# Kernel tuning notes

Measured on AMD Instinct MI355X. Metric: run time of the kernel, lower is better.

Reference implementation:

```python
import jax, jax.numpy as jnp
import numpy as np

N_NODES = 50000
N_EDGES = 800000
IN_DIM = 128
FEAT = 64
HID = 64
OUT = 64
EA_DIM = 3  # edge_attr columns; concat -> weight in_dim = 3*channels


def _uniform(key, shape, lo=-1.0, hi=1.0):
    return jax.random.uniform(key, shape, jnp.float32, lo, hi)


def setup_inputs() -> dict:
    key = jax.random.key(0)
    ks = jax.random.split(key, 12)
    x = jax.random.normal(ks[0], (N_NODES, IN_DIM), jnp.float32)
    edge_index = jax.random.randint(ks[1], (2, N_EDGES), 0, N_NODES, jnp.int32)
    edge_attr = jax.random.uniform(ks[2], (N_EDGES, EA_DIM), jnp.float32)
    # linear_pre (nn.Linear default init approximated; values irrelevant for correctness)
    pre_w = _uniform(ks[3], (IN_DIM, FEAT), -0.08, 0.08)
    pre_b = _uniform(ks[4], (FEAT,), -0.08, 0.08)
    # SAGEConvEGNN weights: uniform(-1, 1), shape [3*in, out]
    w1 = _uniform(ks[5], (EA_DIM * FEAT, HID))
    b1 = _uniform(ks[6], (HID,))
    w2 = _uniform(ks[7], (EA_DIM * HID, HID))
    b2 = _uniform(ks[8], (HID,))
    w3 = _uniform(ks[9], (EA_DIM * HID, OUT))
    b3 = _uniform(ks[10], (OUT,))
    return {"x": x, "edge_index": edge_index, "edge_attr": edge_attr,
            "pre_w": pre_w, "pre_b": pre_b,
            "w1": w1, "b1": b1, "w2": w2, "b2": b2, "w3": w3, "b3": b3}


def _sage_conv(h, src, tgt, edge_attr, w, b, n_nodes):
    # message: x_j scaled by each of the 3 edge_attr columns, concatenated -> [E, 3*C]
    xj = h[src]                                              # gather [E, C]
    msg = (edge_attr[:, :, None] * xj[:, None, :]).reshape(xj.shape[0], -1)
    s = jax.ops.segment_sum(msg, tgt, num_segments=n_nodes)  # scatter-sum [N, 3C]
    cnt = jax.ops.segment_sum(jnp.ones((src.shape[0],), msg.dtype), tgt,
                              num_segments=n_nodes)
    agg = s / jnp.maximum(cnt, 1.0)[:, None]                 # mean; 0 for isolated nodes
    return agg @ w + b


def reference(x, edge_index, edge_attr, pre_w, pre_b, w1, b1, w2, b2, w3, b3):
    src, tgt = edge_index[0], edge_index[1]  # message from j=src aggregated at i=tgt
    n = x.shape[0]
    h = x @ pre_w + pre_b                     # linear_pre
    h = jax.nn.relu(_sage_conv(h, src, tgt, edge_attr, w1, b1, n))
    h = jax.nn.relu(_sage_conv(h, src, tgt, edge_attr, w2, b2, n))
    h = _sage_conv(h, src, tgt, edge_attr, w3, b3, n)
    # F.normalize(p=2, dim=-1) with eps=1e-12
    norm = jnp.sqrt(jnp.sum(h * h, axis=-1, keepdims=True))
    return h / jnp.maximum(norm, 1e-12)
```

## Files before the change

### kernel.cpp

```cpp
#include <hip/hip_runtime.h>
#include <hip/hip_bf16.h>

#define NN 50000
#define NE 800000
#define IND 128
#define C 64
#define NBUCK 196

typedef __hip_bfloat16 bf16;
typedef __attribute__((ext_vector_type(8))) short s8v;
typedef __attribute__((ext_vector_type(4))) float f4v;

__device__ __forceinline__ float to_f(float v) { return v; }
__device__ __forceinline__ float to_f(bf16 v)  { return __bfloat162float(v); }

__device__ __forceinline__ unsigned short f2b(float v) {
    unsigned u = __float_as_uint(v);
    return (unsigned short)((u + 0x7FFFu + ((u >> 16) & 1u)) >> 16);
}
__device__ __forceinline__ float b2f(unsigned short u) {
    return __uint_as_float((unsigned)u << 16);
}

__global__ void detect_kernel(const unsigned* __restrict__ xu, int* __restrict__ flag) {
    int lane = threadIdx.x;
    unsigned u  = xu[lane];
    unsigned ex = (u >> 7) & 0xFF;
    int vote = (ex >= 90 && ex <= 144) ? 1 : 0;
#pragma unroll
    for (int off = 32; off; off >>= 1) vote += __shfl_xor(vote, off, 64);
    if (lane == 0) *flag = (vote < 40) ? 1 : 0;
}

__global__ void count_kernel(const int* __restrict__ tgt, int* __restrict__ cnt) {
    int e = blockIdx.x * blockDim.x + threadIdx.x;
    if (e < NE) atomicAdd(&cnt[tgt[e]], 1);
}

__global__ __launch_bounds__(256) void scanA_kernel(const int4* __restrict__ cnt4,
                                                    int* __restrict__ bsum) {
    __shared__ int ws[4];
    int tid = threadIdx.x;
    int idx = blockIdx.x * 256 + tid;
    int4 v = (idx < NN / 4) ? cnt4[idx] : make_int4(0, 0, 0, 0);
    int s = v.x + v.y + v.z + v.w;
#pragma unroll
    for (int o = 32; o; o >>= 1) s += __shfl_xor(s, o, 64);
    if ((tid & 63) == 0) ws[tid >> 6] = s;
    __syncthreads();
    if (tid == 0) bsum[blockIdx.x] = ws[0] + ws[1] + ws[2] + ws[3];
}

__global__ __launch_bounds__(256) void scanC_kernel(const int4* __restrict__ cnt4,
                                                    const int* __restrict__ bsum,
                                                    int* __restrict__ off) {
    __shared__ int wsum[4];
    int tid = threadIdx.x, lane = tid & 63, wv = tid >> 6;
    int b = blockIdx.x;
    int bb = (lane < b) ? bsum[lane] : 0;
#pragma unroll
    for (int o = 32; o; o >>= 1) bb += __shfl_xor(bb, o, 64);
    int idx = b * 256 + tid;
    int4 v = (idx < NN / 4) ? cnt4[idx] : make_int4(0, 0, 0, 0);
    int tot = v.x + v.y + v.z + v.w;
    int incl = tot;
#pragma unroll
    for (int d = 1; d < 64; d <<= 1) { int t = __shfl_up(incl, d, 64); if (lane >= d) incl += t; }
    if (lane == 63) wsum[wv] = incl;
    __syncthreads();
    int wbase = 0;
#pragma unroll
    for (int j = 0; j < 4; ++j) wbase += (j < wv) ? wsum[j] : 0;
    int excl = bb + wbase + incl - tot;
    if (idx < NN / 4) {
        off[4 * idx]     = excl;
        off[4 * idx + 1] = excl + v.x;
        off[4 * idx + 2] = excl + v.x + v.y;
        off[4 * idx + 3] = excl + v.x + v.y + v.z;
    }
    if (b == 0 && tid == 0) off[NN] = NE;
}

template <typename T>
__device__ __forceinline__ void binA_impl(int* lcnt, int* lbase,
                                          const int* __restrict__ src,
                                          const int* __restrict__ tgt,
                                          const T* __restrict__ ea,
                                          const int* __restrict__ off,
                                          int* __restrict__ ccur,
                                          float4* __restrict__ stg) {
    int tid = threadIdx.x;
    for (int i = tid; i < NBUCK; i += 256) lcnt[i] = 0;
    __syncthreads();
    int e0 = blockIdx.x * 2048;
    float ex[8], ey[8], ez[8];
    unsigned ew[8];
    int eb[8], er[8];
#pragma unroll
    for (int k = 0; k < 8; ++k) {
        int e = e0 + (k << 8) + tid;
        if (e < NE) {
            int t = tgt[e];
            int s = src[e];
            eb[k] = t >> 8;
            ew[k] = ((unsigned)t << 16) | (unsigned)s;
            ex[k] = to_f(ea[e * 3 + 0]);
            ey[k] = to_f(ea[e * 3 + 1]);
            ez[k] = to_f(ea[e * 3 + 2]);
            er[k] = atomicAdd(&lcnt[eb[k]], 1);
        } else eb[k] = -1;
    }
    __syncthreads();
    for (int i = tid; i < NBUCK; i += 256) {
        int c = lcnt[i];
        int g = c ? atomicAdd(&ccur[i], c) : 0;
        lbase[i] = off[i << 8] + g;
    }
    __syncthreads();
#pragma unroll
    for (int k = 0; k < 8; ++k) {
        if (eb[k] >= 0) {
            float4 r;
            r.x = ex[k]; r.y = ey[k]; r.z = ez[k];
            r.w = __uint_as_float(ew[k]);
            stg[lbase[eb[k]] + er[k]] = r;
        }
    }
}

__global__ __launch_bounds__(256) void binA_kernel(const int* __restrict__ src,
                                                   const int* __restrict__ tgt,
                                                   const void* ea,
                                                   const int* __restrict__ off,
                                                   const int* __restrict__ flagp,
                                                   int* __restrict__ ccur,
                                                   float4* __restrict__ stg) {
    __shared__ int lcnt[NBUCK];
    __shared__ int lbase[NBUCK];
    if (*flagp) binA_impl<float>(lcnt, lbase, src, tgt, (const float*)ea, off, ccur, stg);
    else        binA_impl<bf16>(lcnt, lbase, src, tgt, (const bf16*)ea, off, ccur, stg);
}

__global__ __launch_bounds__(256) void binB_kernel(const float4* __restrict__ stg,
                                                   const int* __restrict__ off,
                                                   float4* __restrict__ edge) {
    __shared__ int lfill[256];
    __shared__ int loff[257];
    int tid = threadIdx.x;
    int n0 = blockIdx.x << 8;
    int nn = min(256, NN - n0);
    for (int i = tid; i < nn; i += 256) lfill[i] = 0;
    for (int i = tid; i <= nn; i += 256) loff[i] = off[n0 + i];
    __syncthreads();
    int cb = loff[0], ce = loff[nn];
    for (int i = cb + tid; i < ce; i += 256) {
        float4 r = stg[i];
        unsigned w = __float_as_uint(r.w);
        int l = (int)(w >> 16) & 255;
        int rk = atomicAdd(&lfill[l], 1);
        r.w = __uint_as_float(w & 0xFFFFu);
        edge[loff[l] + rk] = r;
    }
}

template <typename T>
__device__ __forceinline__ void wprep_impl(const T* __restrict__ w, int nT,
                                           unsigned short* __restrict__ oh,
                                           unsigned short* __restrict__ ol) {
    int idx = blockIdx.x * 256 + threadIdx.x;
    if (idx >= 2048 * nT) return;
    int j    = idx & 7;
    int lane = (idx >> 3) & 63;
    int r2   = idx >> 9;
    int t    = r2 % nT;
    int ct   = r2 / nT;
    int k    = 32 * t + ((lane >> 4) << 3) + j;
    int col  = 16 * ct + (lane & 15);
    if constexpr (sizeof(T) == 4) {
        float v = ((const float*)w)[k * 64 + col];
        unsigned short hi = f2b(v);
        oh[idx] = hi;
        ol[idx] = f2b(v - b2f(hi));
    } else {
        oh[idx] = ((const unsigned short*)w)[k * 64 + col];
    }
}

__global__ void wprep_kernel(const void* w, const int* __restrict__ flagp, int nT,
                             unsigned short* __restrict__ oh, unsigned short* __restrict__ ol) {
    if (*flagp) wprep_impl<float>((const float*)w, nT, oh, ol);
    else        wprep_impl<bf16>((const bf16*)w, nT, oh, ol);
}

template <typename T>
__device__ __forceinline__ void preM_impl(const T* __restrict__ x,
                                          const unsigned short* __restrict__ wfh,
                                          const unsigned short* __restrict__ wfl,
                                          const T* __restrict__ b,
                                          unsigned short* __restrict__ h) {
    int tid = threadIdx.x;
    int nb  = blockIdx.x * 64;
    int lane = tid & 63, wv = tid >> 6;
    int m = lane & 15, g = lane >> 4;
    int arow = nb + wv * 16 + m;
    bool okrow = arow < NN;
    f4v acc[4] = {};
    for (int t = 0; t < 4; ++t) {
        if constexpr (sizeof(T) == 4) {
            float av[8];
            if (okrow) {
                const float* xr = (const float*)x + (size_t)arow * IND + t * 32 + g * 8;
                float4 v0 = *(const float4*)xr;
                float4 v1 = *(const float4*)(xr + 4);
                av[0] = v0.x; av[1] = v0.y; av[2] = v0.z; av[3] = v0.w;
                av[4] = v1.x; av[5] = v1.y; av[6] = v1.z; av[7] = v1.w;
            } else {
#pragma unroll
                for (int j = 0; j < 8; ++j) av[j] = 0.f;
            }
            s8v ahi, alo;
#pragma unroll
            for (int j = 0; j < 8; ++j) {
                unsigned short hi = f2b(av[j]);
                ahi[j] = (short)hi;
                alo[j] = (short)f2b(av[j] - b2f(hi));
            }
#pragma unroll
            for (int ct = 0; ct < 4; ++ct) {
                int fo = ((ct * 4 + t) * 64 + lane) * 8;
                s8v bh = *(const s8v*)&wfh[fo];
                s8v bl = *(const s8v*)&wfl[fo];
                acc[ct] = __builtin_amdgcn_mfma_f32_16x16x32_bf16(ahi, bh, acc[ct], 0, 0, 0);
                acc[ct] = __builtin_amdgcn_mfma_f32_16x16x32_bf16(alo, bh, acc[ct], 0, 0, 0);
                acc[ct] = __builtin_amdgcn_mfma_f32_16x16x32_bf16(ahi, bl, acc[ct], 0, 0, 0);
            }
        } else {
            s8v ahi = {};
            if (okrow)
                ahi = *(const s8v*)((const unsigned short*)x + (size_t)arow * IND + t * 32 + g * 8);
#pragma unroll
            for (int ct = 0; ct < 4; ++ct) {
                int fo = ((ct * 4 + t) * 64 + lane) * 8;
                s8v bh = *(const s8v*)&wfh[fo];
                acc[ct] = __builtin_amdgcn_mfma_f32_16x16x32_bf16(ahi, bh, acc[ct], 0, 0, 0);
            }
        }
    }
#pragma unroll
    for (int r = 0; r < 4; ++r) {
        int drow = nb + wv * 16 + g * 4 + r;
        if (drow < NN) {
#pragma unroll
            for (int ct = 0; ct < 4; ++ct)
                h[(size_t)drow * C + 16 * ct + m] = f2b(acc[ct][r] + to_f(b[16 * ct + m]));
        }
    }
}

__global__ __launch_bounds__(256) void preM_kernel(const void* x,
                                                   const unsigned short* __restrict__ wfh,
                                                   const unsigned short* __restrict__ wfl,
                                                   const void* b, const int* __restrict__ flagp,
                                                   unsigned short* __restrict__ h) {
    if (*flagp) preM_impl<float>((const float*)x, wfh, wfl, (const float*)b, h);
    else        preM_impl<bf16>((const bf16*)x, wfh, wfl, (const bf16*)b, h);
}

__global__ __launch_bounds__(256) void agg_kernel(const unsigned short* __restrict__ hb,
                                                  const float4* __restrict__ edge,
                                                  const int* __restrict__ off,
                                                  float* __restrict__ s) {
    int f = threadIdx.x & 63;
    int n = blockIdx.x * 4 + (threadIdx.x >> 6);
    int beg = __builtin_amdgcn_readfirstlane(off[n]);
    int end = __builtin_amdgcn_readfirstlane(off[n + 1]);
    float a0 = 0.f, a1 = 0.f, a2 = 0.f;
    int cnt = end - beg;
    int m4 = beg + (cnt & ~3);
    int e = beg;
    if (beg + 8 <= m4) {
        float4 c0 = edge[e],     c1 = edge[e + 1], c2 = edge[e + 2], c3 = edge[e + 3];
        float4 d0 = edge[e + 4], d1 = edge[e + 5], d2 = edge[e + 6], d3 = edge[e + 7];
        float h0 = b2f(hb[(__float_as_int(c0.w) << 6) + f]);
        float h1 = b2f(hb[(__float_as_int(c1.w) << 6) + f]);
        float h2 = b2f(hb[(__float_as_int(c2.w) << 6) + f]);
        float h3 = b2f(hb[(__float_as_int(c3.w) << 6) + f]);
        int e2 = beg + 8;
        while (e2 < m4) {
            float g0 = b2f(hb[(__float_as_int(d0.w) << 6) + f]);
            float g1 = b2f(hb[(__float_as_int(d1.w) << 6) + f]);
            float g2 = b2f(hb[(__float_as_int(d2.w) << 6) + f]);
            float g3 = b2f(hb[(__float_as_int(d3.w) << 6) + f]);
            float4 n0 = edge[e2], n1 = edge[e2 + 1], n2 = edge[e2 + 2], n3 = edge[e2 + 3];
            a0 += c0.x * h0; a1 += c0.y * h0; a2 += c0.z * h0;
            a0 += c1.x * h1; a1 += c1.y * h1; a2 += c1.z * h1;
            a0 += c2.x * h2; a1 += c2.y * h2; a2 += c2.z * h2;
            a0 += c3.x * h3; a1 += c3.y * h3; a2 += c3.z * h3;
            c0 = d0; c1 = d1; c2 = d2; c3 = d3;
            h0 = g0; h1 = g1; h2 = g2; h3 = g3;
            d0 = n0; d1 = n1; d2 = n2; d3 = n3;
            e2 += 4;
        }
        float g0 = b2f(hb[(__float_as_int(d0.w) << 6) + f]);
        float g1 = b2f(hb[(__float_as_int(d1.w) << 6) + f]);
        float g2 = b2f(hb[(__float_as_int(d2.w) << 6) + f]);
        float g3 = b2f(hb[(__float_as_int(d3.w) << 6) + f]);
        a0 += c0.x * h0; a1 += c0.y * h0; a2 += c0.z * h0;
        a0 += c1.x * h1; a1 += c1.y * h1; a2 += c1.z * h1;
        a0 += c2.x * h2; a1 += c2.y * h2; a2 += c2.z * h2;
        a0 += c3.x * h3; a1 += c3.y * h3; a2 += c3.z * h3;
        a0 += d0.x * g0; a1 += d0.y * g0; a2 += d0.z * g0;
        a0 += d1.x * g1; a1 += d1.y * g1; a2 += d1.z * g1;
        a0 += d2.x * g2; a1 += d2.y * g2; a2 += d2.z * g2;
        a0 += d3.x * g3; a1 += d3.y * g3; a2 += d3.z * g3;
        e = m4;
    } else if (beg + 4 <= m4) {
        float4 c0 = edge[e], c1 = edge[e + 1], c2 = edge[e + 2], c3 = edge[e + 3];
        float h0 = b2f(hb[(__float_as_int(c0.w) << 6) + f]);
        float h1 = b2f(hb[(__float_as_int(c1.w) << 6) + f]);
        float h2 = b2f(hb[(__float_as_int(c2.w) << 6) + f]);
        float h3 = b2f(hb[(__float_as_int(c3.w) << 6) + f]);
        a0 += c0.x * h0; a1 += c0.y * h0; a2 += c0.z * h0;
        a0 += c1.x * h1; a1 += c1.y * h1; a2 += c1.z * h1;
        a0 += c2.x * h2; a1 += c2.y * h2; a2 += c2.z * h2;
        a0 += c3.x * h3; a1 += c3.y * h3; a2 += c3.z * h3;
        e = m4;
    }
    for (; e < end; ++e) {
        float4 r = edge[e];
        float hv = b2f(hb[(__float_as_int(r.w) << 6) + f]);
        a0 += r.x * hv; a1 += r.y * hv; a2 += r.z * hv;
    }
    float iv = 1.0f / fmaxf((float)cnt, 1.0f);
    float* so = s + n * 192;
    so[f] = a0 * iv; so[64 + f] = a1 * iv; so[128 + f] = a2 * iv;
}

template <typename T, int MODE>
__device__ __forceinline__ void gemmM_impl(const float* __restrict__ s,
                                           const unsigned short* __restrict__ wfh,
                                           const unsigned short* __restrict__ wfl,
                                           const T* __restrict__ b,
                                           unsigned short* __restrict__ hout, T* __restrict__ out) {
    int tid = threadIdx.x;
    int nb  = blockIdx.x * 64;
    int lane = tid & 63, wv = tid >> 6;
    int m = lane & 15, g = lane >> 4;
    int arow = nb + wv * 16 + m;
    bool okrow = arow < NN;
    const float* srow = s + (size_t)arow * 192 + g * 8;
    f4v acc[4] = {};
    for (int t = 0; t < 6; ++t) {
        float av[8];
        if (okrow) {
            float4 v0 = *(const float4*)(srow + t * 32);
            float4 v1 = *(const float4*)(srow + t * 32 + 4);
            av[0] = v0.x; av[1] = v0.y; av[2] = v0.z; av[3] = v0.w;
            av[4] = v1.x; av[5] = v1.y; av[6] = v1.z; av[7] = v1.w;
        } else {
#pragma unroll
            for (int j = 0; j < 8; ++j) av[j] = 0.f;
        }
        s8v ahi, alo;
#pragma unroll
        for (int j = 0; j < 8; ++j) {
            unsigned short hi = f2b(av[j]);
            ahi[j] = (short)hi;
            alo[j] = (short)f2b(av[j] - b2f(hi));
        }
#pragma unroll
        for (int ct = 0; ct < 4; ++ct) {
            int fo = ((ct * 6 + t) * 64 + lane) * 8;
            s8v bh = *(const s8v*)&wfh[fo];
            acc[ct] = __builtin_amdgcn_mfma_f32_16x16x32_bf16(ahi, bh, acc[ct], 0, 0, 0);
            acc[ct] = __builtin_amdgcn_mfma_f32_16x16x32_bf16(alo, bh, acc[ct], 0, 0, 0);
            if constexpr (sizeof(T) == 4) {
                s8v bl = *(const s8v*)&wfl[fo];
                acc[ct] = __builtin_amdgcn_mfma_f32_16x16x32_bf16(ahi, bl, acc[ct], 0, 0, 0);
            }
        }
    }
    float vv[4][4];
#pragma unroll
    for (int ct = 0; ct < 4; ++ct) {
        float bv = to_f(b[16 * ct + m]);
#pragma unroll
        for (int r = 0; r < 4; ++r) vv[ct][r] = acc[ct][r] + bv;
    }
    if constexpr (MODE == 0) {
#pragma unroll
        for (int r = 0; r < 4; ++r) {
            int drow = nb + wv * 16 + g * 4 + r;
            if (drow < NN) {
#pragma unroll
                for (int ct = 0; ct < 4; ++ct)
                    hout[(size_t)drow * C + 16 * ct + m] = f2b(fmaxf(vv[ct][r], 0.f));
            }
        }
    } else {
#pragma unroll
        for (int r = 0; r < 4; ++r) {
            float sq = vv[0][r] * vv[0][r] + vv[1][r] * vv[1][r]
                     + vv[2][r] * vv[2][r] + vv[3][r] * vv[3][r];
#pragma unroll
            for (int o = 1; o < 16; o <<= 1) sq += __shfl_xor(sq, o, 64);
            float innorm = 1.0f / fmaxf(sqrtf(sq), 1e-12f);
            int drow = nb + wv * 16 + g * 4 + r;
            if (drow < NN) {
#pragma unroll
                for (int ct = 0; ct < 4; ++ct) {
                    float rv = vv[ct][r] * innorm;
                    if constexpr (sizeof(T) == 2) out[(size_t)drow * C + 16 * ct + m] = __float2bfloat16(rv);
                    else                          out[(size_t)drow * C + 16 * ct + m] = rv;
                }
            }
        }
    }
}

__global__ __launch_bounds__(256) void gemm_relu(const float* __restrict__ s,
                                                 const unsigned short* __restrict__ wfh,
                                                 const unsigned short* __restrict__ wfl,
                                                 const void* b, const int* __restrict__ flagp,
                                                 unsigned short* __restrict__ hout) {
    if (*flagp) gemmM_impl<float, 0>(s, wfh, wfl, (const float*)b, hout, (float*)nullptr);
    else        gemmM_impl<bf16, 0>(s, wfh, wfl, (const bf16*)b, hout, (bf16*)nullptr);
}

__global__ __launch_bounds__(256) void gemm_norm(const float* __restrict__ s,
                                                 const unsigned short* __restrict__ wfh,
                                                 const unsigned short* __restrict__ wfl,
                                                 const void* b, const int* __restrict__ flagp,
                                                 void* out) {
    if (*flagp) gemmM_impl<float, 1>(s, wfh, wfl, (const float*)b, nullptr, (float*)out);
    else        gemmM_impl<bf16, 1>(s, wfh, wfl, (const bf16*)b, nullptr, (bf16*)out);
}

extern "C" void kernel_launch(void* const* d_in, const int* in_sizes, int n_in,
                              void* d_out, int out_size, void* d_ws, size_t ws_size,
                              hipStream_t stream) {
    const void* x     = d_in[0];
    const int*  ei    = (const int*)d_in[1];
    const void* ea    = d_in[2];
    const void* pre_w = d_in[3];
    const void* pre_b = d_in[4];
    const void* W[3]  = {d_in[5], d_in[7], d_in[9]};
    const void* B[3]  = {d_in[6], d_in[8], d_in[10]};
    const int* src = ei;
    const int* tgt = ei + NE;

    float4*         EDGE = (float4*)d_ws;
    float*          S    = (float*)(EDGE + NE);
    float4*         STG  = (float4*)S;
    unsigned short* H    = (unsigned short*)(S + (size_t)NN * 192);
    int*            CNT  = (int*)(H + (size_t)NN * C);
    int*            CCUR = CNT + NN;
    int*            OFF  = CCUR + 256;
    int*            BSUM = OFF + NN + 8;
    int*            FLAG = BSUM + 64;
    unsigned short* WPH  = (unsigned short*)(FLAG + 16);
    unsigned short* WPL  = WPH + 8192;
    unsigned short* WFH  = WPL + 8192;
    unsigned short* WFL  = WFH + 3 * 12288;

    detect_kernel<<<1, 64, 0, stream>>>((const unsigned*)x, FLAG);
    wprep_kernel<<<32, 256, 0, stream>>>(pre_w, FLAG, 4, WPH, WPL);
    for (int l = 0; l < 3; ++l)
        wprep_kernel<<<48, 256, 0, stream>>>(W[l], FLAG, 6, WFH + l * 12288, WFL + l * 12288);
    hipMemsetAsync(CNT, 0, (NN + 256) * sizeof(int), stream);
    count_kernel<<<(NE + 255) / 256, 256, 0, stream>>>(tgt, CNT);
    scanA_kernel<<<(NN / 4 + 255) / 256, 256, 0, stream>>>((const int4*)CNT, BSUM);
    scanC_kernel<<<(NN / 4 + 255) / 256, 256, 0, stream>>>((const int4*)CNT, BSUM, OFF);
    binA_kernel<<<(NE + 2047) / 2048, 256, 0, stream>>>(src, tgt, ea, OFF, FLAG, CCUR, STG);
    binB_kernel<<<NBUCK, 256, 0, stream>>>(STG, OFF, EDGE);
    preM_kernel<<<(NN + 63) / 64, 256, 0, stream>>>(x, WPH, WPL, pre_b, FLAG, H);

    int nblk = (NN + 63) / 64;
    for (int l = 0; l < 3; ++l) {
        agg_kernel<<<NN / 4, 256, 0, stream>>>(H, EDGE, OFF, S);
        if (l < 2)
            gemm_relu<<<nblk, 256, 0, stream>>>(S, WFH + l * 12288, WFL + l * 12288, B[l], FLAG, H);
        else
            gemm_norm<<<nblk, 256, 0, stream>>>(S, WFH + l * 12288, WFL + l * 12288, B[l], FLAG, d_out);
    }
}
```

Baseline: 317.9 us.

## Fuse preprocessing kernels, derive CSR offsets in bucket pass, store agg as bf16 pairs

Merges the weight-prep launches with a per-bucket target count into one kernel. It replaces the per-node count plus two-stage scan with a tiny bucket scan, and computes the per-node CSR offsets inside the binB pass, which is fused with the pre-linear GEMM. The aggregation now writes hi/lo bf16 splits instead of fp32, so the GEMM loads them directly without converting. This cuts the number of launches and removes the global per-node atomics, at the cost of an extra pass over staging in binB and more complex shared-memory logic.

```diff
diff --git a/kernel.cpp b/kernel.cpp
--- a/kernel.cpp
+++ b/kernel.cpp
@@ -32,38 +32,55 @@
     if (lane == 0) *flag = (vote < 40) ? 1 : 0;
 }
 
-__global__ void count_kernel(const int* __restrict__ tgt, int* __restrict__ cnt) {
-    int e = blockIdx.x * blockDim.x + threadIdx.x;
-    if (e < NE) atomicAdd(&cnt[tgt[e]], 1);
-}
-
-__global__ __launch_bounds__(256) void scanA_kernel(const int4* __restrict__ cnt4,
-                                                    int* __restrict__ bsum) {
-    __shared__ int ws[4];
+__global__ __launch_bounds__(256) void prep_kernel(const void* pw, const void* w0,
+        const void* w1, const void* w2, const int* __restrict__ flagp,
+        const int* __restrict__ tgt,
+        unsigned short* __restrict__ oh, unsigned short* __restrict__ ol,
+        int* __restrict__ bcnt) {
+    __shared__ int lc[NBUCK];
+    int blk = blockIdx.x;
     int tid = threadIdx.x;
-    int idx = blockIdx.x * 256 + tid;
-    int4 v = (idx < NN / 4) ? cnt4[idx] : make_int4(0, 0, 0, 0);
-    int s = v.x + v.y + v.z + v.w;
-#pragma unroll
-    for (int o = 32; o; o >>= 1) s += __shfl_xor(s, o, 64);
-    if ((tid & 63) == 0) ws[tid >> 6] = s;
-    __syncthreads();
-    if (tid == 0) bsum[blockIdx.x] = ws[0] + ws[1] + ws[2] + ws[3];
-}
-
-__global__ __launch_bounds__(256) void scanC_kernel(const int4* __restrict__ cnt4,
-                                                    const int* __restrict__ bsum,
+    if (blk < 176) {
+        int gid = blk * 256 + tid;
+        const void* w; int nT, idx, base;
+        if (gid < 8192) { w = pw; nT = 4; idx = gid; base = 0; }
+        else {
+            int r = gid - 8192; int l = r / 12288; idx = r % 12288; nT = 6;
+            w = (l == 0) ? w0 : (l == 1) ? w1 : w2; base = 8192 + l * 12288;
+        }
+        int j = idx & 7, lane = (idx >> 3) & 63, r2 = idx >> 9;
+        int t = r2 % nT, ct = r2 / nT;
+        int k = 32 * t + ((lane >> 4) << 3) + j;
+        int col = 16 * ct + (lane & 15);
+        if (*flagp) {
+            float v = ((const float*)w)[k * 64 + col];
+            unsigned short hi = f2b(v);
+            oh[base + idx] = hi;
+            ol[base + idx] = f2b(v - b2f(hi));
+        } else {
+            oh[base + idx] = ((const unsigned short*)w)[k * 64 + col];
+        }
+    } else {
+        for (int i = tid; i < NBUCK; i += 256) lc[i] = 0;
+        __syncthreads();
+        int e0 = (blk - 176) * 2048;
+#pragma unroll
+        for (int k = 0; k < 8; ++k) {
+            int e = e0 + (k << 8) + tid;
+            if (e < NE) atomicAdd(&lc[tgt[e] >> 8], 1);
+        }
+        __syncthreads();
+        for (int i = tid; i < NBUCK; i += 256) if (lc[i]) atomicAdd(&bcnt[i], lc[i]);
+    }
+}
+
+__global__ __launch_bounds__(256) void bscan_kernel(const int* __restrict__ bcnt,
+                                                    int* __restrict__ boff,
                                                     int* __restrict__ off) {
     __shared__ int wsum[4];
     int tid = threadIdx.x, lane = tid & 63, wv = tid >> 6;
-    int b = blockIdx.x;
-    int bb = (lane < b) ? bsum[lane] : 0;
-#pragma unroll
-    for (int o = 32; o; o >>= 1) bb += __shfl_xor(bb, o, 64);
-    int idx = b * 256 + tid;
-    int4 v = (idx < NN / 4) ? cnt4[idx] : make_int4(0, 0, 0, 0);
-    int tot = v.x + v.y + v.z + v.w;
-    int incl = tot;
+    int v = (tid < NBUCK) ? bcnt[tid] : 0;
+    int incl = v;
 #pragma unroll
     for (int d = 1; d < 64; d <<= 1) { int t = __shfl_up(incl, d, 64); if (lane >= d) incl += t; }
     if (lane == 63) wsum[wv] = incl;
@@ -71,14 +88,8 @@
     int wbase = 0;
 #pragma unroll
     for (int j = 0; j < 4; ++j) wbase += (j < wv) ? wsum[j] : 0;
-    int excl = bb + wbase + incl - tot;
-    if (idx < NN / 4) {
-        off[4 * idx]     = excl;
-        off[4 * idx + 1] = excl + v.x;
-        off[4 * idx + 2] = excl + v.x + v.y;
-        off[4 * idx + 3] = excl + v.x + v.y + v.z;
-    }
-    if (b == 0 && tid == 0) off[NN] = NE;
+    if (tid < NBUCK) boff[tid] = wbase + incl - v;
+    if (tid == 0) { boff[NBUCK] = NE; off[NN] = NE; }
 }
 
 template <typename T>
@@ -86,7 +97,7 @@
                                           const int* __restrict__ src,
                                           const int* __restrict__ tgt,
                                           const T* __restrict__ ea,
-                                          const int* __restrict__ off,
+                                          const int* __restrict__ boff,
                                           int* __restrict__ ccur,
                                           float4* __restrict__ stg) {
     int tid = threadIdx.x;
@@ -114,7 +125,7 @@
     for (int i = tid; i < NBUCK; i += 256) {
         int c = lcnt[i];
         int g = c ? atomicAdd(&ccur[i], c) : 0;
-        lbase[i] = off[i << 8] + g;
+        lbase[i] = boff[i] + g;
     }
     __syncthreads();
 #pragma unroll
@@ -131,75 +142,23 @@
 __global__ __launch_bounds__(256) void binA_kernel(const int* __restrict__ src,
                                                    const int* __restrict__ tgt,
                                                    const void* ea,
-                                                   const int* __restrict__ off,
+                                                   const int* __restrict__ boff,
                                                    const int* __restrict__ flagp,
                                                    int* __restrict__ ccur,
                                                    float4* __restrict__ stg) {
     __shared__ int lcnt[NBUCK];
     __shared__ int lbase[NBUCK];
-    if (*flagp) binA_impl<float>(lcnt, lbase, src, tgt, (const float*)ea, off, ccur, stg);
-    else        binA_impl<bf16>(lcnt, lbase, src, tgt, (const bf16*)ea, off, ccur, stg);
-}
-
-__global__ __launch_bounds__(256) void binB_kernel(const float4* __restrict__ stg,
-                                                   const int* __restrict__ off,
-                                                   float4* __restrict__ edge) {
-    __shared__ int lfill[256];
-    __shared__ int loff[257];
-    int tid = threadIdx.x;
-    int n0 = blockIdx.x << 8;
-    int nn = min(256, NN - n0);
-    for (int i = tid; i < nn; i += 256) lfill[i] = 0;
-    for (int i = tid; i <= nn; i += 256) loff[i] = off[n0 + i];
-    __syncthreads();
-    int cb = loff[0], ce = loff[nn];
-    for (int i = cb + tid; i < ce; i += 256) {
-        float4 r = stg[i];
-        unsigned w = __float_as_uint(r.w);
-        int l = (int)(w >> 16) & 255;
-        int rk = atomicAdd(&lfill[l], 1);
-        r.w = __uint_as_float(w & 0xFFFFu);
-        edge[loff[l] + rk] = r;
-    }
+    if (*flagp) binA_impl<float>(lcnt, lbase, src, tgt, (const float*)ea, boff, ccur, stg);
+    else        binA_impl<bf16>(lcnt, lbase, src, tgt, (const bf16*)ea, boff, ccur, stg);
 }
 
 template <typename T>
-__device__ __forceinline__ void wprep_impl(const T* __restrict__ w, int nT,
-                                           unsigned short* __restrict__ oh,
-                                           unsigned short* __restrict__ ol) {
-    int idx = blockIdx.x * 256 + threadIdx.x;
-    if (idx >= 2048 * nT) return;
-    int j    = idx & 7;
-    int lane = (idx >> 3) & 63;
-    int r2   = idx >> 9;
-    int t    = r2 % nT;
-    int ct   = r2 / nT;
-    int k    = 32 * t + ((lane >> 4) << 3) + j;
-    int col  = 16 * ct + (lane & 15);
-    if constexpr (sizeof(T) == 4) {
-        float v = ((const float*)w)[k * 64 + col];
-        unsigned short hi = f2b(v);
-        oh[idx] = hi;
-        ol[idx] = f2b(v - b2f(hi));
-    } else {
-        oh[idx] = ((const unsigned short*)w)[k * 64 + col];
-    }
-}
-
-__global__ void wprep_kernel(const void* w, const int* __restrict__ flagp, int nT,
-                             unsigned short* __restrict__ oh, unsigned short* __restrict__ ol) {
-    if (*flagp) wprep_impl<float>((const float*)w, nT, oh, ol);
-    else        wprep_impl<bf16>((const bf16*)w, nT, oh, ol);
-}
-
-template <typename T>
-__device__ __forceinline__ void preM_impl(const T* __restrict__ x,
+__device__ __forceinline__ void preM_body(int nb, const T* __restrict__ x,
                                           const unsigned short* __restrict__ wfh,
                                           const unsigned short* __restrict__ wfl,
                                           const T* __restrict__ b,
                                           unsigned short* __restrict__ h) {
     int tid = threadIdx.x;
-    int nb  = blockIdx.x * 64;
     int lane = tid & 63, wv = tid >> 6;
     int m = lane & 15, g = lane >> 4;
     int arow = nb + wv * 16 + m;
@@ -257,19 +216,62 @@
     }
 }
 
-__global__ __launch_bounds__(256) void preM_kernel(const void* x,
-                                                   const unsigned short* __restrict__ wfh,
-                                                   const unsigned short* __restrict__ wfl,
-                                                   const void* b, const int* __restrict__ flagp,
-                                                   unsigned short* __restrict__ h) {
-    if (*flagp) preM_impl<float>((const float*)x, wfh, wfl, (const float*)b, h);
-    else        preM_impl<bf16>((const bf16*)x, wfh, wfl, (const bf16*)b, h);
+__global__ __launch_bounds__(256) void binB_pre_kernel(const float4* __restrict__ stg,
+        const int* __restrict__ boff, int* __restrict__ off, float4* __restrict__ edge,
+        const void* x, const unsigned short* __restrict__ wfh,
+        const unsigned short* __restrict__ wfl, const void* pb,
+        const int* __restrict__ flagp, unsigned short* __restrict__ h) {
+    __shared__ int lcnt[256];
+    __shared__ int lexcl[256];
+    __shared__ int lfill[256];
+    __shared__ int wsum[4];
+    int tid = threadIdx.x;
+    if (blockIdx.x < NBUCK) {
+        int b = blockIdx.x;
+        int n0 = b << 8;
+        int cb = boff[b], ce = boff[b + 1];
+        lcnt[tid] = 0;
+        __syncthreads();
+        for (int i = cb + tid; i < ce; i += 256) {
+            unsigned w = __float_as_uint(stg[i].w);
+            atomicAdd(&lcnt[(w >> 16) & 255], 1);
+        }
+        __syncthreads();
+        int lane = tid & 63, wv = tid >> 6;
+        int v = lcnt[tid];
+        int incl = v;
+#pragma unroll
+        for (int d = 1; d < 64; d <<= 1) { int t = __shfl_up(incl, d, 64); if (lane >= d) incl += t; }
+        if (lane == 63) wsum[wv] = incl;
+        __syncthreads();
+        int wbase = 0;
+#pragma unroll
+        for (int j = 0; j < 4; ++j) wbase += (j < wv) ? wsum[j] : 0;
+        lexcl[tid] = wbase + incl - v;
+        lfill[tid] = 0;
+        __syncthreads();
+        int n = n0 + tid;
+        if (n <= NN) off[n] = cb + lexcl[tid];
+        for (int i = cb + tid; i < ce; i += 256) {
+            float4 r = stg[i];
+            unsigned w = __float_as_uint(r.w);
+            int l = (int)(w >> 16) & 255;
+            int rk = atomicAdd(&lfill[l], 1);
+            r.w = __uint_as_float(w & 0xFFFFu);
+            edge[cb + lexcl[l] + rk] = r;
+        }
+    } else {
+        int nb = (blockIdx.x - NBUCK) * 64;
+        if (*flagp) preM_body<float>(nb, (const float*)x, wfh, wfl, (const float*)pb, h);
+        else        preM_body<bf16>(nb, (const bf16*)x, wfh, wfl, (const bf16*)pb, h);
+    }
 }
 
 __global__ __launch_bounds__(256) void agg_kernel(const unsigned short* __restrict__ hb,
                                                   const float4* __restrict__ edge,
                                                   const int* __restrict__ off,
-                                                  float* __restrict__ s) {
+                                                  unsigned short* __restrict__ sh,
+                                                  unsigned short* __restrict__ sl) {
     int f = threadIdx.x & 63;
     int n = blockIdx.x * 4 + (threadIdx.x >> 6);
     int beg = __builtin_amdgcn_readfirstlane(off[n]);
@@ -332,12 +334,17 @@
         a0 += r.x * hv; a1 += r.y * hv; a2 += r.z * hv;
     }
     float iv = 1.0f / fmaxf((float)cnt, 1.0f);
-    float* so = s + n * 192;
-    so[f] = a0 * iv; so[64 + f] = a1 * iv; so[128 + f] = a2 * iv;
+    size_t base = (size_t)n * 192;
+    float v0 = a0 * iv, v1 = a1 * iv, v2 = a2 * iv;
+    unsigned short x0 = f2b(v0), x1 = f2b(v1), x2 = f2b(v2);
+    sh[base + f]       = x0; sl[base + f]       = f2b(v0 - b2f(x0));
+    sh[base + 64 + f]  = x1; sl[base + 64 + f]  = f2b(v1 - b2f(x1));
+    sh[base + 128 + f] = x2; sl[base + 128 + f] = f2b(v2 - b2f(x2));
 }
 
 template <typename T, int MODE>
-__device__ __forceinline__ void gemmM_impl(const float* __restrict__ s,
+__device__ __forceinline__ void gemmM_impl(const unsigned short* __restrict__ sh,
+                                           const unsigned short* __restrict__ sl,
                                            const unsigned short* __restrict__ wfh,
                                            const unsigned short* __restrict__ wfl,
                                            const T* __restrict__ b,
@@ -348,25 +355,14 @@
     int m = lane & 15, g = lane >> 4;
     int arow = nb + wv * 16 + m;
     bool okrow = arow < NN;
-    const float* srow = s + (size_t)arow * 192 + g * 8;
+    const unsigned short* shrow = sh + (size_t)arow * 192 + g * 8;
+    const unsigned short* slrow = sl + (size_t)arow * 192 + g * 8;
     f4v acc[4] = {};
     for (int t = 0; t < 6; ++t) {
-        float av[8];
+        s8v ahi = {}, alo = {};
         if (okrow) {
-            float4 v0 = *(const float4*)(srow + t * 32);
-            float4 v1 = *(const float4*)(srow + t * 32 + 4);
-            av[0] = v0.x; av[1] = v0.y; av[2] = v0.z; av[3] = v0.w;
-            av[4] = v1.x; av[5] = v1.y; av[6] = v1.z; av[7] = v1.w;
-        } else {
-#pragma unroll
-            for (int j = 0; j < 8; ++j) av[j] = 0.f;
-        }
-        s8v ahi, alo;
-#pragma unroll
-        for (int j = 0; j < 8; ++j) {
-            unsigned short hi = f2b(av[j]);
-            ahi[j] = (short)hi;
-            alo[j] = (short)f2b(av[j] - b2f(hi));
+            ahi = *(const s8v*)(shrow + t * 32);
+            alo = *(const s8v*)(slrow + t * 32);
         }
 #pragma unroll
         for (int ct = 0; ct < 4; ++ct) {
@@ -418,22 +414,24 @@
     }
 }
 
-__global__ __launch_bounds__(256) void gemm_relu(const float* __restrict__ s,
+__global__ __launch_bounds__(256) void gemm_relu(const unsigned short* __restrict__ sh,
+                                                 const unsigned short* __restrict__ sl,
                                                  const unsigned short* __restrict__ wfh,
                                                  const unsigned short* __restrict__ wfl,
                                                  const void* b, const int* __restrict__ flagp,
                                                  unsigned short* __restrict__ hout) {
-    if (*flagp) gemmM_impl<float, 0>(s, wfh, wfl, (const float*)b, hout, (float*)nullptr);
-    else        gemmM_impl<bf16, 0>(s, wfh, wfl, (const bf16*)b, hout, (bf16*)nullptr);
-}
-
-__global__ __launch_bounds__(256) void gemm_norm(const float* __restrict__ s,
+    if (*flagp) gemmM_impl<float, 0>(sh, sl, wfh, wfl, (const float*)b, hout, (float*)nullptr);
+    else        gemmM_impl<bf16, 0>(sh, sl, wfh, wfl, (const bf16*)b, hout, (bf16*)nullptr);
+}
+
+__global__ __launch_bounds__(256) void gemm_norm(const unsigned short* __restrict__ sh,
+                                                 const unsigned short* __restrict__ sl,
                                                  const unsigned short* __restrict__ wfh,
                                                  const unsigned short* __restrict__ wfl,
                                                  const void* b, const int* __restrict__ flagp,
                                                  void* out) {
-    if (*flagp) gemmM_impl<float, 1>(s, wfh, wfl, (const float*)b, nullptr, (float*)out);
-    else        gemmM_impl<bf16, 1>(s, wfh, wfl, (const bf16*)b, nullptr, (bf16*)out);
+    if (*flagp) gemmM_impl<float, 1>(sh, sl, wfh, wfl, (const float*)b, nullptr, (float*)out);
+    else        gemmM_impl<bf16, 1>(sh, sl, wfh, wfl, (const bf16*)b, nullptr, (bf16*)out);
 }
 
 extern "C" void kernel_launch(void* const* d_in, const int* in_sizes, int n_in,
@@ -450,37 +448,35 @@
     const int* tgt = ei + NE;
 
     float4*         EDGE = (float4*)d_ws;
-    float*          S    = (float*)(EDGE + NE);
-    float4*         STG  = (float4*)S;
-    unsigned short* H    = (unsigned short*)(S + (size_t)NN * 192);
-    int*            CNT  = (int*)(H + (size_t)NN * C);
-    int*            CCUR = CNT + NN;
-    int*            OFF  = CCUR + 256;
-    int*            BSUM = OFF + NN + 8;
-    int*            FLAG = BSUM + 64;
-    unsigned short* WPH  = (unsigned short*)(FLAG + 16);
-    unsigned short* WPL  = WPH + 8192;
-    unsigned short* WFH  = WPL + 8192;
-    unsigned short* WFL  = WFH + 3 * 12288;
-
+    unsigned short* SH   = (unsigned short*)(EDGE + NE);
+    unsigned short* SL   = SH + (size_t)NN * 192;
+    float4*         STG  = (float4*)SH;
+    unsigned short* H    = SL + (size_t)NN * 192;
+    int*            BCNT = (int*)(H + (size_t)NN * C);
+    int*            CCUR = BCNT + 256;
+    int*            BOFF = CCUR + 256;
+    int*            OFF  = BOFF + 256;
+    int*            FLAG = OFF + NN + 8;
+    unsigned short* WH   = (unsigned short*)(FLAG + 16);
+    unsigned short* WL   = WH + 45056;
+
+    hipMemsetAsync(BCNT, 0, 512 * sizeof(int), stream);
     detect_kernel<<<1, 64, 0, stream>>>((const unsigned*)x, FLAG);
-    wprep_kernel<<<32, 256, 0, stream>>>(pre_w, FLAG, 4, WPH, WPL);
-    for (int l = 0; l < 3; ++l)
-        wprep_kernel<<<48, 256, 0, stream>>>(W[l], FLAG, 6, WFH + l * 12288, WFL + l * 12288);
-    hipMemsetAsync(CNT, 0, (NN + 256) * sizeof(int), stream);
-    count_kernel<<<(NE + 255) / 256, 256, 0, stream>>>(tgt, CNT);
-    scanA_kernel<<<(NN / 4 + 255) / 256, 256, 0, stream>>>((const int4*)CNT, BSUM);
-    scanC_kernel<<<(NN / 4 + 255) / 256, 256, 0, stream>>>((const int4*)CNT, BSUM, OFF);
-    binA_kernel<<<(NE + 2047) / 2048, 256, 0, stream>>>(src, tgt, ea, OFF, FLAG, CCUR, STG);
-    binB_kernel<<<NBUCK, 256, 0, stream>>>(STG, OFF, EDGE);
-    preM_kernel<<<(NN + 63) / 64, 256, 0, stream>>>(x, WPH, WPL, pre_b, FLAG, H);
+    prep_kernel<<<176 + (NE + 2047) / 2048, 256, 0, stream>>>(pre_w, W[0], W[1], W[2],
+                                                              FLAG, tgt, WH, WL, BCNT);
+    bscan_kernel<<<1, 256, 0, stream>>>(BCNT, BOFF, OFF);
+    binA_kernel<<<(NE + 2047) / 2048, 256, 0, stream>>>(src, tgt, ea, BOFF, FLAG, CCUR, STG);
+    binB_pre_kernel<<<NBUCK + (NN + 63) / 64, 256, 0, stream>>>(STG, BOFF, OFF, EDGE,
+                                                                x, WH, WL, pre_b, FLAG, H);
 
     int nblk = (NN + 63) / 64;
     for (int l = 0; l < 3; ++l) {
-        agg_kernel<<<NN / 4, 256, 0, stream>>>(H, EDGE, OFF, S);
+        const unsigned short* wfh = WH + 8192 + l * 12288;
+        const unsigned short* wfl = WL + 8192 + l * 12288;
+        agg_kernel<<<NN / 4, 256, 0, stream>>>(H, EDGE, OFF, SH, SL);
         if (l < 2)
-            gemm_relu<<<nblk, 256, 0, stream>>>(S, WFH + l * 12288, WFL + l * 12288, B[l], FLAG, H);
+            gemm_relu<<<nblk, 256, 0, stream>>>(SH, SL, wfh, wfl, B[l], FLAG, H);
         else
-            gemm_norm<<<nblk, 256, 0, stream>>>(S, WFH + l * 12288, WFL + l * 12288, B[l], FLAG, d_out);
-    }
-}
+            gemm_norm<<<nblk, 256, 0, stream>>>(SH, SL, wfh, wfl, B[l], FLAG, d_out);
+    }
+}
```

New measurement: 278.2 us. 1.14x faster.
